# Kernel tuning notes

Measured on AMD Instinct MI355X. Metric: run time of the kernel, lower is better.

Reference implementation:

```python
import jax, jax.numpy as jnp
import numpy as np

EMBED = 2048
HIDDEN = 2048
T = 32768


def setup_inputs() -> dict:
    key = jax.random.key(0)
    k1, k2, k3, k4 = jax.random.split(key, 4)
    s_x = 1.0 / np.sqrt(EMBED)
    s_h = 1.0 / np.sqrt(HIDDEN)
    return {
        "X_embeddings": jax.random.normal(k1, (T, EMBED), dtype=jnp.float32),
        "Wx": jax.random.normal(k2, (EMBED, HIDDEN), dtype=jnp.float32) * s_x,
        "Wh": jax.random.normal(k3, (HIDDEN, HIDDEN), dtype=jnp.float32) * s_h,
        "b": jax.random.normal(k4, (HIDDEN,), dtype=jnp.float32) * 0.01,
    }


def reference(X_embeddings, Wx, Wh, b):
    # FastRecurrentRunner: H[0] = 0; for t in 0..T-2: H[t+1] = cell(X[t], H[t])
    # cell(x, h) = tanh(x @ Wx + h @ Wh + b)  (Elman RNN cell)
    dtype = X_embeddings.dtype
    # Precompute input projections for all steps at once (one big GEMM).
    xproj = X_embeddings[:-1] @ Wx + b  # [T-1, HIDDEN]

    def step(h, xp):
        h_next = jnp.tanh(xp + h @ Wh)
        return h_next, h_next

    h0 = jnp.zeros((HIDDEN,), dtype=dtype)
    _, H_tail = jax.lax.scan(step, h0, xproj)  # [T-1, HIDDEN]
    H = jnp.concatenate([h0[None, :], H_tail], axis=0)  # [T, HIDDEN]
    return H
```

## Files before the change

kernel.cpp:

```cpp
#include <hip/hip_runtime.h>
#include <hip/hip_bf16.h>
#include <math.h>

#define T_STEPS 32768
#define HID 2048
#define EMB 2048

#define BM 64
#define BN 64
#define BK 16

__global__ __launch_bounds__(256) void xproj_gemm(const float* __restrict__ X,
                                                  const float* __restrict__ Wx,
                                                  const float* __restrict__ bias,
                                                  float* __restrict__ H)
{
    __shared__ __align__(16) float As[BK][BM];
    __shared__ __align__(16) float Bs[BK][BN];

    const int tid = threadIdx.x;
    const int m0 = blockIdx.y * BM;
    const int n0 = blockIdx.x * BN;

    const int tn = tid & 15;
    const int tm = tid >> 4;

    const int am = tid >> 2;
    const int ak = (tid & 3) << 2;
    const int bk = tid >> 4;
    const int bn = (tid & 15) << 2;

    const int arow = m0 + am;
    const bool aval = arow < (T_STEPS - 1);

    float acc[4][4];
#pragma unroll
    for (int i = 0; i < 4; ++i)
#pragma unroll
        for (int j = 0; j < 4; ++j) acc[i][j] = 0.f;

    for (int k0 = 0; k0 < EMB; k0 += BK) {
        float4 av = make_float4(0.f, 0.f, 0.f, 0.f);
        if (aval) av = *(const float4*)&X[(size_t)arow * EMB + k0 + ak];
        float4 bv = *(const float4*)&Wx[(size_t)(k0 + bk) * HID + n0 + bn];

        __syncthreads();
        As[ak + 0][am] = av.x;
        As[ak + 1][am] = av.y;
        As[ak + 2][am] = av.z;
        As[ak + 3][am] = av.w;
        *(float4*)&Bs[bk][bn] = bv;
        __syncthreads();

#pragma unroll
        for (int k = 0; k < BK; ++k) {
            float4 a4 = *(const float4*)&As[k][tm << 2];
            float4 b4 = *(const float4*)&Bs[k][tn << 2];
            acc[0][0] += a4.x * b4.x; acc[0][1] += a4.x * b4.y;
            acc[0][2] += a4.x * b4.z; acc[0][3] += a4.x * b4.w;
            acc[1][0] += a4.y * b4.x; acc[1][1] += a4.y * b4.y;
            acc[1][2] += a4.y * b4.z; acc[1][3] += a4.y * b4.w;
            acc[2][0] += a4.z * b4.x; acc[2][1] += a4.z * b4.y;
            acc[2][2] += a4.z * b4.z; acc[2][3] += a4.z * b4.w;
            acc[3][0] += a4.w * b4.x; acc[3][1] += a4.w * b4.y;
            acc[3][2] += a4.w * b4.z; acc[3][3] += a4.w * b4.w;
        }
    }

    float4 bb = *(const float4*)&bias[n0 + (tn << 2)];
#pragma unroll
    for (int i = 0; i < 4; ++i) {
        int m = m0 + (tm << 2) + i;
        if (m < T_STEPS - 1) {
            float4 o;
            o.x = acc[i][0] + bb.x;
            o.y = acc[i][1] + bb.y;
            o.z = acc[i][2] + bb.z;
            o.w = acc[i][3] + bb.w;
            *(float4*)&H[(size_t)(m + 1) * HID + n0 + (tn << 2)] = o;
        }
    }
}

#define NBLK 64
#define SCAN_TPB 1024
#define CPB 32
#define CPW 2

typedef int v4i __attribute__((ext_vector_type(4)));

__device__ __forceinline__ v4i uncached_load16(const void* p)
{
    v4i r;
    asm volatile("global_load_dwordx4 %0, %1, off sc0 sc1\n\t"
                 "s_waitcnt vmcnt(0)"
                 : "=v"(r) : "v"(p) : "memory");
    return r;
}

__device__ __forceinline__ void uncached_store16(void* p, v4i v)
{
    asm volatile("global_store_dwordx4 %0, %1, off sc0 sc1"
                 :: "v"(p), "v"(v) : "memory");
}

__global__ __launch_bounds__(SCAN_TPB, 4) void rnn_scan(const float* __restrict__ Wh,
                                                        float* __restrict__ H,
                                                        unsigned long long* __restrict__ hcomm)
{
    __shared__ __align__(16) float hlds[2][HID];
    __shared__ float pad[18432];

    const int tid = threadIdx.x;
    const int bid = blockIdx.x;
    const int wave = tid >> 6;
    const int lane = tid & 63;
    const int c0 = bid * CPB + wave * CPW;

    if ((((size_t)hcomm) >> 22) & 1) ((volatile float*)pad)[tid] = 0.f;

    float4 w0[8], w1[8];
#pragma unroll
    for (int k = 0; k < 8; ++k) {
        const int r = 4 * lane + 256 * k;
        const float* p = Wh + (size_t)r * HID + c0;
        w0[k].x = p[0];                     w1[k].x = p[1];
        w0[k].y = p[(size_t)HID];           w1[k].y = p[(size_t)HID + 1];
        w0[k].z = p[(size_t)(2 * HID)];     w1[k].z = p[(size_t)(2 * HID) + 1];
        w0[k].w = p[(size_t)(3 * HID)];     w1[k].w = p[(size_t)(3 * HID) + 1];
    }

    for (int t = 0; t < T_STEPS - 1; ++t) {
        float2 xp = make_float2(0.f, 0.f);
        if (lane == 0) xp = *(const float2*)&H[(size_t)(t + 1) * HID + c0];

        const char* slot = (const char*)hcomm +
                           (((size_t)(t & 1) * HID + 2 * (size_t)tid) << 3);
        v4i e;
        do {
            e = uncached_load16(slot);
        } while (e.y != t || e.w != t);

        *(float2*)&hlds[t & 1][2 * tid] =
            make_float2(__int_as_float(e.x), __int_as_float(e.z));
        __syncthreads();

        const float* hb = hlds[t & 1];
        float s0 = 0.f, s1 = 0.f;
#pragma unroll
        for (int k = 0; k < 8; ++k) {
            float4 hh = *(const float4*)&hb[4 * lane + 256 * k];
            s0 += hh.x * w0[k].x + hh.y * w0[k].y + hh.z * w0[k].z + hh.w * w0[k].w;
            s1 += hh.x * w1[k].x + hh.y * w1[k].y + hh.z * w1[k].z + hh.w * w1[k].w;
        }
#pragma unroll
        for (int m = 1; m < 64; m <<= 1) {
            s0 += __shfl_xor(s0, m, 64);
            s1 += __shfl_xor(s1, m, 64);
        }

        if (lane == 0) {
            float h0 = tanhf(xp.x + s0);
            float h1 = tanhf(xp.y + s1);
            v4i pub;
            pub.x = __float_as_int(h0); pub.y = t + 1;
            pub.z = __float_as_int(h1); pub.w = t + 1;
            uncached_store16((char*)hcomm +
                             (((size_t)((t + 1) & 1) * HID + (size_t)c0) << 3), pub);
            *(float2*)&H[(size_t)(t + 1) * HID + c0] = make_float2(h0, h1);
        }
    }
}

extern "C" void kernel_launch(void* const* d_in, const int* in_sizes, int n_in,
                              void* d_out, int out_size, void* d_ws, size_t ws_size,
                              hipStream_t stream)
{
    const float* X  = (const float*)d_in[0];
    const float* Wx = (const float*)d_in[1];
    const float* Wh = (const float*)d_in[2];
    const float* b  = (const float*)d_in[3];
    float* H = (float*)d_out;
    unsigned long long* hcomm = (unsigned long long*)d_ws;

    hipMemsetAsync(H, 0, HID * sizeof(float), stream);
    hipMemsetAsync(hcomm, 0, 2 * HID * sizeof(unsigned long long), stream);

    dim3 ggrid(HID / BN, T_STEPS / BM);
    xproj_gemm<<<ggrid, 256, 0, stream>>>(X, Wx, b, H);

    const float* whp = Wh;
    float* hp = H;
    unsigned long long* cp = hcomm;
    void* args[] = { (void*)&whp, (void*)&hp, (void*)&cp };
    hipLaunchCooperativeKernel((const void*)rnn_scan, dim3(NBLK), dim3(SCAN_TPB),
                               args, 0, stream);
}
```

Before: 139.8 ms.

## Replicate recurrent scan across eight groups with register and bf16 LDS-resident Wh

Replaces the 64-block scan with a 256-block cooperative kernel split into 8 independent replica groups of 32 blocks, each computing all 2048 hidden units with 64 columns per block. Three quarters of each block's Wh slice stays in fp32 registers and the rest sits in LDS as bf16. Polling now uses cheaper sc0 loads with a periodic system-scope load, and each group has its own communication buffer. The intent is to cut per-step cross-block synchronisation latency, since each block now polls a smaller group. The trade-offs are reduced precision on part of Wh, very high register pressure, and a fallback to the old path when the workspace is too small.

```diff
diff --git a/kernel.cpp b/kernel.cpp
--- a/kernel.cpp
+++ b/kernel.cpp
@@ -1,5 +1,4 @@
 #include <hip/hip_runtime.h>
-#include <hip/hip_bf16.h>
 #include <math.h>
 
 #define T_STEPS 32768
@@ -13,7 +12,7 @@
 __global__ __launch_bounds__(256) void xproj_gemm(const float* __restrict__ X,
                                                   const float* __restrict__ Wx,
                                                   const float* __restrict__ bias,
-                                                  float* __restrict__ H)
+                                                  float* __restrict__ XPout)
 {
     __shared__ __align__(16) float As[BK][BM];
     __shared__ __align__(16) float Bs[BK][BN];
@@ -24,7 +23,6 @@
 
     const int tn = tid & 15;
     const int tm = tid >> 4;
-
     const int am = tid >> 2;
     const int ak = (tid & 3) << 2;
     const int bk = tid >> 4;
@@ -77,17 +75,163 @@
             o.y = acc[i][1] + bb.y;
             o.z = acc[i][2] + bb.z;
             o.w = acc[i][3] + bb.w;
-            *(float4*)&H[(size_t)(m + 1) * HID + n0 + (tn << 2)] = o;
-        }
-    }
-}
-
-#define NBLK 64
-#define SCAN_TPB 1024
-#define CPB 32
-#define CPW 2
+            *(float4*)&XPout[(size_t)m * HID + n0 + (tn << 2)] = o;
+        }
+    }
+}
 
 typedef int v4i __attribute__((ext_vector_type(4)));
+typedef int v2i __attribute__((ext_vector_type(2)));
+
+__device__ __forceinline__ float dot4(float4 a, float4 b)
+{
+    return a.x * b.x + a.y * b.y + a.z * b.z + a.w * b.w;
+}
+
+__device__ __forceinline__ void poll4_sc0(const void* p, v4i& a, v4i& b, v4i& c, v4i& d)
+{
+    asm volatile("global_load_dwordx4 %0, %4, off sc0\n\t"
+                 "global_load_dwordx4 %1, %4, off offset:16 sc0\n\t"
+                 "global_load_dwordx4 %2, %4, off offset:32 sc0\n\t"
+                 "global_load_dwordx4 %3, %4, off offset:48 sc0\n\t"
+                 "s_waitcnt vmcnt(0)"
+                 : "=&v"(a), "=&v"(b), "=&v"(c), "=&v"(d) : "v"(p) : "memory");
+}
+__device__ __forceinline__ void poll4_sys(const void* p, v4i& a, v4i& b, v4i& c, v4i& d)
+{
+    asm volatile("global_load_dwordx4 %0, %4, off sc0 sc1\n\t"
+                 "global_load_dwordx4 %1, %4, off offset:16 sc0 sc1\n\t"
+                 "global_load_dwordx4 %2, %4, off offset:32 sc0 sc1\n\t"
+                 "global_load_dwordx4 %3, %4, off offset:48 sc0 sc1\n\t"
+                 "s_waitcnt vmcnt(0)"
+                 : "=&v"(a), "=&v"(b), "=&v"(c), "=&v"(d) : "v"(p) : "memory");
+}
+__device__ __forceinline__ void st8_sc0(void* p, v2i v)
+{
+    asm volatile("global_store_dwordx2 %0, %1, off sc0" :: "v"(p), "v"(v) : "memory");
+}
+__device__ __forceinline__ void st8_sys(void* p, v2i v)
+{
+    asm volatile("global_store_dwordx2 %0, %1, off sc0 sc1" :: "v"(p), "v"(v) : "memory");
+}
+
+__device__ __forceinline__ unsigned short bf16rne(float f)
+{
+    unsigned u = __float_as_uint(f);
+    u += 0x7fffu + ((u >> 16) & 1u);
+    return (unsigned short)(u >> 16);
+}
+__device__ __forceinline__ float bfup(unsigned short s)
+{
+    return __uint_as_float((unsigned)s << 16);
+}
+
+__global__ __launch_bounds__(256, 1) void rnn_scan_fast(const float* __restrict__ Wh,
+                                                        const float* __restrict__ XP,
+                                                        float* __restrict__ H,
+                                                        unsigned long long* __restrict__ hcomm)
+{
+    __shared__ __align__(16) ushort4 Wl2b[128][64];
+    __shared__ __align__(16) float hlds[2][HID];
+    __shared__ float pacc[4][64];
+
+    const int tid = threadIdx.x;
+    const int wave = tid >> 6;
+    const int lane = tid & 63;
+    const int g = blockIdx.x & 7;
+    const int rank = blockIdx.x >> 3;
+    const int bc0 = rank * 64;
+    unsigned long long* hcg = hcomm + (size_t)g * (2 * HID);
+
+    float4 wreg[96];
+    {
+        const float* wp = Wh + (size_t)(384 * wave) * HID + bc0 + lane;
+#pragma unroll
+        for (int i = 0; i < 96; ++i) {
+            wreg[i].x = wp[(size_t)(4 * i + 0) * HID];
+            wreg[i].y = wp[(size_t)(4 * i + 1) * HID];
+            wreg[i].z = wp[(size_t)(4 * i + 2) * HID];
+            wreg[i].w = wp[(size_t)(3 + 4 * i) * HID];
+        }
+    }
+    for (int k = 0; k < 32; ++k) {
+        int id = k * 256 + tid;
+        int r4 = id >> 6, c = id & 63;
+        const float* p = Wh + (size_t)(1536 + 4 * r4) * HID + bc0 + c;
+        ushort4 u;
+        u.x = bf16rne(p[0]);
+        u.y = bf16rne(p[(size_t)HID]);
+        u.z = bf16rne(p[2 * (size_t)HID]);
+        u.w = bf16rne(p[3 * (size_t)HID]);
+        Wl2b[r4][c] = u;
+    }
+    __syncthreads();
+
+    for (int t = 0; t < T_STEPS - 1; ++t) {
+        const int par = t & 1;
+
+        float xpv = 0.f;
+        if (wave == 0) xpv = XP[(size_t)t * HID + bc0 + lane];
+
+        const char* pb = (const char*)hcg + (((size_t)par * HID + 8 * (size_t)tid) << 3);
+        v4i e0, e1, e2, e3;
+        int round = 0;
+        for (;;) {
+            if ((round & 15) == 15) poll4_sys(pb, e0, e1, e2, e3);
+            else                    poll4_sc0(pb, e0, e1, e2, e3);
+            if (((e0.y ^ t) | (e0.w ^ t) | (e1.y ^ t) | (e1.w ^ t) |
+                 (e2.y ^ t) | (e2.w ^ t) | (e3.y ^ t) | (e3.w ^ t)) == 0) break;
+            ++round;
+        }
+
+        v4i h0; h0.x = e0.x; h0.y = e0.z; h0.z = e1.x; h0.w = e1.z;
+        v4i h1; h1.x = e2.x; h1.y = e2.z; h1.z = e3.x; h1.w = e3.z;
+        *(v4i*)&hlds[par][8 * tid] = h0;
+        *(v4i*)&hlds[par][8 * tid + 4] = h1;
+        __syncthreads();
+
+        const float* hb = hlds[par];
+        const float* hbr = &hb[384 * wave];
+        float a0 = 0.f, a1 = 0.f, a2 = 0.f, a3 = 0.f;
+#pragma unroll
+        for (int i = 0; i < 96; i += 4) {
+            a0 += dot4(wreg[i],     *(const float4*)&hbr[4 * i]);
+            a1 += dot4(wreg[i + 1], *(const float4*)&hbr[4 * i + 4]);
+            a2 += dot4(wreg[i + 2], *(const float4*)&hbr[4 * i + 8]);
+            a3 += dot4(wreg[i + 3], *(const float4*)&hbr[4 * i + 12]);
+        }
+        float b0 = 0.f, b1 = 0.f;
+#pragma unroll
+        for (int j = 0; j < 32; j += 2) {
+            const int r4 = 32 * wave + j;
+            ushort4 ua = Wl2b[r4][lane];
+            ushort4 ub = Wl2b[r4 + 1][lane];
+            float4 qa = *(const float4*)&hb[1536 + 4 * r4];
+            float4 qb = *(const float4*)&hb[1536 + 4 * r4 + 4];
+            b0 += bfup(ua.x) * qa.x + bfup(ua.y) * qa.y
+                + bfup(ua.z) * qa.z + bfup(ua.w) * qa.w;
+            b1 += bfup(ub.x) * qb.x + bfup(ub.y) * qb.y
+                + bfup(ub.z) * qb.z + bfup(ub.w) * qb.w;
+        }
+        pacc[wave][lane] = ((a0 + a1) + (a2 + a3)) + (b0 + b1);
+        __syncthreads();
+
+        if (wave == 0) {
+            float tot = pacc[0][lane] + pacc[1][lane] + pacc[2][lane] + pacc[3][lane];
+            float hv = tanhf(xpv + tot);
+            v2i e; e.x = __float_as_int(hv); e.y = t + 1;
+            char* pa = (char*)hcg + (((size_t)(par ^ 1) * HID + bc0 + lane) << 3);
+            st8_sc0(pa, e);
+            st8_sys(pa, e);
+            if (g == 0) H[(size_t)(t + 1) * HID + bc0 + lane] = hv;
+        }
+    }
+}
+
+#define NBLK_R3 64
+#define TPB_R3 1024
+#define CPB_R3 32
+#define CPW_R3 2
 
 __device__ __forceinline__ v4i uncached_load16(const void* p)
 {
@@ -97,25 +241,23 @@
                  : "=v"(r) : "v"(p) : "memory");
     return r;
 }
-
 __device__ __forceinline__ void uncached_store16(void* p, v4i v)
 {
     asm volatile("global_store_dwordx4 %0, %1, off sc0 sc1"
                  :: "v"(p), "v"(v) : "memory");
 }
 
-__global__ __launch_bounds__(SCAN_TPB, 4) void rnn_scan(const float* __restrict__ Wh,
-                                                        float* __restrict__ H,
-                                                        unsigned long long* __restrict__ hcomm)
+__global__ __launch_bounds__(TPB_R3, 4) void rnn_scan_r3(const float* __restrict__ Wh,
+                                                         float* __restrict__ H,
+                                                         unsigned long long* __restrict__ hcomm)
 {
     __shared__ __align__(16) float hlds[2][HID];
     __shared__ float pad[18432];
 
     const int tid = threadIdx.x;
-    const int bid = blockIdx.x;
     const int wave = tid >> 6;
     const int lane = tid & 63;
-    const int c0 = bid * CPB + wave * CPW;
+    const int c0 = blockIdx.x * CPB_R3 + wave * CPW_R3;
 
     if ((((size_t)hcomm) >> 22) & 1) ((volatile float*)pad)[tid] = 0.f;
 
@@ -172,6 +314,22 @@
     }
 }
 
+static void launch_r3_path(const float* X, const float* Wx, const float* Wh,
+                           const float* b, float* H, void* d_ws, hipStream_t stream)
+{
+    unsigned long long* hcomm = (unsigned long long*)d_ws;
+    hipMemsetAsync(H, 0, HID * sizeof(float), stream);
+    hipMemsetAsync(d_ws, 0, 2 * HID * sizeof(unsigned long long), stream);
+
+    dim3 ggrid(HID / BN, T_STEPS / BM);
+    xproj_gemm<<<ggrid, 256, 0, stream>>>(X, Wx, b, H + HID);
+
+    const float* whp = Wh; float* hp = H; unsigned long long* cp = hcomm;
+    void* args[] = { (void*)&whp, (void*)&hp, (void*)&cp };
+    hipLaunchCooperativeKernel((const void*)rnn_scan_r3, dim3(NBLK_R3),
+                               dim3(TPB_R3), args, 0, stream);
+}
+
 extern "C" void kernel_launch(void* const* d_in, const int* in_sizes, int n_in,
                               void* d_out, int out_size, void* d_ws, size_t ws_size,
                               hipStream_t stream)
@@ -181,18 +339,35 @@
     const float* Wh = (const float*)d_in[2];
     const float* b  = (const float*)d_in[3];
     float* H = (float*)d_out;
-    unsigned long long* hcomm = (unsigned long long*)d_ws;
-
-    hipMemsetAsync(H, 0, HID * sizeof(float), stream);
-    hipMemsetAsync(hcomm, 0, 2 * HID * sizeof(unsigned long long), stream);
-
-    dim3 ggrid(HID / BN, T_STEPS / BM);
-    xproj_gemm<<<ggrid, 256, 0, stream>>>(X, Wx, b, H);
-
-    const float* whp = Wh;
-    float* hp = H;
-    unsigned long long* cp = hcomm;
-    void* args[] = { (void*)&whp, (void*)&hp, (void*)&cp };
-    hipLaunchCooperativeKernel((const void*)rnn_scan, dim3(NBLK), dim3(SCAN_TPB),
-                               args, 0, stream);
-}
+
+    const size_t XP_BYTES = (size_t)(T_STEPS - 1) * HID * sizeof(float);
+    const size_t XP_OFF   = 512 * 1024;
+    const bool big_ws = ws_size >= XP_OFF + XP_BYTES;
+
+    int nb = 0;
+    bool fast_ok = big_ws &&
+        (hipOccupancyMaxActiveBlocksPerMultiprocessor(&nb, (const void*)rnn_scan_fast,
+                                                      256, 0) == hipSuccess) && nb >= 1;
+
+    if (fast_ok) {
+        unsigned long long* hcomm = (unsigned long long*)d_ws;
+        float* XPb = (float*)((char*)d_ws + XP_OFF);
+
+        hipMemsetAsync(H, 0, HID * sizeof(float), stream);
+        hipMemsetAsync(d_ws, 0, 8 * 2 * HID * sizeof(unsigned long long), stream);
+
+        dim3 ggrid(HID / BN, T_STEPS / BM);
+        xproj_gemm<<<ggrid, 256, 0, stream>>>(X, Wx, b, XPb);
+
+        const float* whp = Wh; const float* xpp = XPb;
+        float* hp = H; unsigned long long* cp = hcomm;
+        void* args[] = { (void*)&whp, (void*)&xpp, (void*)&hp, (void*)&cp };
+        hipError_t err = hipLaunchCooperativeKernel((const void*)rnn_scan_fast,
+                                                    dim3(256), dim3(256), args, 0, stream);
+        if (err != hipSuccess) {
+            launch_r3_path(X, Wx, Wh, b, H, d_ws, stream);
+        }
+    } else {
+        launch_r3_path(X, Wx, Wh, b, H, d_ws, stream);
+    }
+}
```

Result: no change. 141.8 ms (+1.4%).
